# Performance work log

Hardware: AMD Instinct MI355X
Metric: run time of the kernel (lower is better)

## Reference

```python
import jax, jax.numpy as jnp
import numpy as np

WINDOW = 60
DEPTH = 3
HIDDEN = 256
LN_EPS = 1e-5


def _lyndon_indices(d):
    # Lyndon words over alphabet {0..d-1}, lengths 2 and 3, lexicographic order
    # (signatory mode='words' extracts expanded-logsig coefficients at Lyndon words).
    i2 = np.array([(i, j) for i in range(d) for j in range(d) if (i, j) < (j, i)], dtype=np.int32)
    i3 = np.array([(i, j, k) for i in range(d) for j in range(d) for k in range(d)
                   if (i, j, k) < (j, k, i) and (i, j, k) < (k, i, j)], dtype=np.int32)
    return i2, i3


def _logsig_features(x):
    # x: [b, s, c] -> logsignature of time-augmented sliding windows: [b*s, sig_channels]
    b, s, c = x.shape
    d = c + 1
    # replicate-padded sliding windows via clipped gather (matches F.pad replicate + unfold)
    pos = jnp.clip(jnp.arange(s)[:, None] + jnp.arange(WINDOW)[None, :] - (WINDOW - 1), 0, s - 1)
    windows = x[:, pos, :]                                   # [b, s, W, c]
    t = jnp.linspace(0.0, 1.0, WINDOW, dtype=x.dtype)        # time augmentation channel
    t_b = jnp.broadcast_to(t[None, None, :, None], (b, s, WINDOW, 1))
    aug = jnp.concatenate([t_b, windows], axis=-1).reshape(b * s, WINDOW, d)
    N = b * s
    # basepoint=True: prepend zero point -> increments include the first point itself
    inc = jnp.diff(aug, axis=1, prepend=jnp.zeros((N, 1, d), aug.dtype))  # [N, W, d]
    inc_t = jnp.transpose(inc, (1, 0, 2))                    # [W, N, d]

    def chen_step(carry, v):
        S1, S2, S3 = carry
        vv = jnp.einsum('ni,nj->nij', v, v)
        vvv = jnp.einsum('nij,nk->nijk', vv, v)
        nS3 = S3 + jnp.einsum('nij,nk->nijk', S2, v) \
                 + 0.5 * jnp.einsum('ni,njk->nijk', S1, vv) + vvv / 6.0
        nS2 = S2 + jnp.einsum('ni,nj->nij', S1, v) + 0.5 * vv
        nS1 = S1 + v
        return (nS1, nS2, nS3), None

    init = (jnp.zeros((N, d), x.dtype), jnp.zeros((N, d, d), x.dtype), jnp.zeros((N, d, d, d), x.dtype))
    (S1, S2, S3), _ = jax.lax.scan(chen_step, init, inc_t)
    # log in truncated tensor algebra: log(1+x) = x - x^2/2 + x^3/3
    L1 = S1
    L2 = S2 - 0.5 * jnp.einsum('ni,nj->nij', S1, S1)
    L3 = (S3 - 0.5 * (jnp.einsum('ni,njk->nijk', S1, S2) + jnp.einsum('nij,nk->nijk', S2, S1))
          + jnp.einsum('ni,nj,nk->nijk', S1, S1, S1) / 3.0)
    i2, i3 = _lyndon_indices(d)
    f2 = L2[:, i2[:, 0], i2[:, 1]]
    f3 = L3[:, i3[:, 0], i3[:, 1], i3[:, 2]]
    return jnp.concatenate([L1, f2, f3], axis=-1)            # [N, sig_channels]


def setup_inputs() -> dict:
    key = jax.random.key(0)
    ks = jax.random.split(key, 5)
    b, s, c = 8, 2048, 8
    d = c + 1
    sig_channels = d + (d * d - d) // 2 + (d ** 3 - d) // 3  # 285 for d=9
    h2 = 2 * HIDDEN
    x = jax.random.normal(ks[0], (b, s, c), dtype=jnp.float32)
    w1 = jax.random.normal(ks[1], (sig_channels, h2), dtype=jnp.float32) / np.sqrt(sig_channels)
    b1 = jnp.zeros((h2,), jnp.float32)
    ln_g = jnp.ones((h2,), jnp.float32)
    ln_b = jnp.zeros((h2,), jnp.float32)
    w2 = jax.random.normal(ks[2], (h2, HIDDEN), dtype=jnp.float32) / np.sqrt(h2)
    b2 = jnp.zeros((HIDDEN,), jnp.float32)
    return {"x": x, "w1": w1, "b1": b1, "ln_g": ln_g, "ln_b": ln_b, "w2": w2, "b2": b2}


def reference(x, w1, b1, ln_g, ln_b, w2, b2):
    b, s, _ = x.shape
    feats = _logsig_features(x)                              # [b*s, sig_channels]
    h = jax.nn.gelu(feats @ w1 + b1, approximate=False)      # torch default GELU (erf)
    mu = jnp.mean(h, axis=-1, keepdims=True)
    var = jnp.var(h, axis=-1, keepdims=True)
    h = (h - mu) / jnp.sqrt(var + LN_EPS) * ln_g + ln_b      # LayerNorm; Dropout is eval no-op
    out = h @ w2 + b2
    return out.reshape(b, s, -1)
```

## Files before the change

kernel.cpp:

```cpp
#include <hip/hip_runtime.h>
#include <hip/hip_bf16.h>
#include <cstdint>
#include <cstddef>

typedef short short8 __attribute__((ext_vector_type(8)));
typedef float f32x4 __attribute__((ext_vector_type(4)));
typedef float f32x2 __attribute__((ext_vector_type(2)));

#define NS    2048
#define KPAD  288
#define H2    512
#define HID   256
#define WPB   7
#define SBLK  293
#define SIGBLKS (8 * SBLK)

#define MFMA(a,b,c) __builtin_amdgcn_mfma_f32_16x16x32_bf16((a),(b),(c),0,0,0)

__device__ __forceinline__ void gl2lds16(const void* g, void* l) {
    __builtin_amdgcn_global_load_lds(
        (const __attribute__((address_space(1))) void*)g,
        (__attribute__((address_space(3))) void*)l, 16, 0, 0);
}
__device__ __forceinline__ float geluf(float x) {
    return 0.5f * x * (1.0f + erff(x * 0.70710678118654752f));
}
__device__ __forceinline__ f32x4 shfl4(f32x4 v, int d) {
    f32x4 r;
    r[0] = __shfl_xor(v[0], d); r[1] = __shfl_xor(v[1], d);
    r[2] = __shfl_xor(v[2], d); r[3] = __shfl_xor(v[3], d);
    return r;
}

struct Tbl3 { short col[729]; };
static constexpr Tbl3 make_tbl3() {
    Tbl3 t{};
    for (int x = 0; x < 729; ++x) t.col[x] = -1;
    int r = 0;
    for (int i = 0; i < 9; ++i)
        for (int j = 0; j < 9; ++j)
            for (int k = 0; k < 9; ++k) {
                bool lt1 = (i < j) || (i == j && (j < k || (j == k && k < i)));
                bool lt2 = (i < k) || (i == k && (j < i || (j == i && k < j)));
                if (lt1 && lt2) { t.col[(i*9+j)*9+k] = (short)(45 + r); ++r; }
            }
    return t;
}
static constexpr Tbl3 TBL3 = make_tbl3();

#define SIG_STEP(VA_,VB_,VC_) { \
    const float hh = 0.5f * S1i + vi * (1.0f/6.0f); \
    const float ra = S2ra + hh * (VA_); \
    const float rb = S2rb + hh * (VB_); \
    const float rc = S2rc + hh * (VC_); \
    const f32x2 ra2 = {ra, ra}, rb2 = {rb, rb}, rc2 = {rc, rc}; \
    S3sa += ra * v0; S3pa0 += ra2*vp0; S3pa1 += ra2*vp1; S3pa2 += ra2*vp2; S3pa3 += ra2*vp3; \
    S3sb += rb * v0; S3pb0 += rb2*vp0; S3pb1 += rb2*vp1; S3pb2 += rb2*vp2; S3pb3 += rb2*vp3; \
    S3sc += rc * v0; S3pc0 += rc2*vp0; S3pc1 += rc2*vp1; S3pc2 += rc2*vp2; S3pc3 += rc2*vp3; \
    const float aa = S1i + 0.5f * vi; \
    S2ra += aa * (VA_); S2rb += aa * (VB_); S2rc += aa * (VC_); \
    S1i += vi; }

#define SIG_DSTEP(E0,E1,RS,VA_,VB_,VC_) { \
    const float4 e0 = (E0); const float4 e1 = (E1); const float rs = (RS); \
    const float v0 = DT; \
    const f32x2 vp0 = {e0.x, e0.y}, vp1 = {e0.z, e0.w}, vp2 = {e1.x, e1.y}, vp3 = {e1.z, e1.w}; \
    const float vi = (ci == 0) ? DT : rs; \
    SIG_STEP(VA_,VB_,VC_) }

#define SIG_MAIN(VA_,VB_,VC_) { \
    { const float* xr = &X[(g0 - lo) * 8]; \
      const float4 e0 = *(const float4*)xr; \
      const float4 e1 = *(const float4*)(xr + 4); \
      const float rs = xr[ioff]; \
      const float v0 = 0.0f; \
      const f32x2 vp0 = {e0.x, e0.y}, vp1 = {e0.z, e0.w}, vp2 = {e1.x, e1.y}, vp3 = {e1.z, e1.w}; \
      const float vi = (ci == 0) ? 0.0f : rs; \
      SIG_STEP(VA_,VB_,VC_) } \
    const float* pd = &PD[(sm59 + 1 - lo + 59) * 8]; \
    float4 p0 = *(const float4*)pd; \
    float4 p1 = *(const float4*)(pd + 4); \
    float  pr = pd[ioff]; \
    float4 q0 = *(const float4*)(pd + 8); \
    float4 q1 = *(const float4*)(pd + 12); \
    float  qr = (pd + 8)[ioff]; \
    _Pragma("unroll 1") \
    for (int j = 1; j < 59; j += 2) { \
      pd += 16; \
      const float4 a0 = *(const float4*)pd; \
      const float4 a1 = *(const float4*)(pd + 4); \
      const float  ar = pd[ioff]; \
      const float4 b0 = *(const float4*)(pd + 8); \
      const float4 b1 = *(const float4*)(pd + 12); \
      const float  br = (pd + 8)[ioff]; \
      SIG_DSTEP(p0, p1, pr, VA_,VB_,VC_) \
      SIG_DSTEP(q0, q1, qr, VA_,VB_,VC_) \
      p0 = a0; p1 = a1; pr = ar; \
      q0 = b0; q1 = b1; qr = br; \
    } \
    SIG_DSTEP(p0, p1, pr, VA_,VB_,VC_) }

#define SIG_ST(RA,RB,RC) \
    if (act) { \
        if ((RA) == 0) S1buf[widx * 9 + ci] = S1i; \
        float* sb = &S2buf[widx * 81 + ci * 9]; \
        sb[RA] = S2ra; sb[RB] = S2rb; sb[RC] = S2rc; \
    }

#define S3EL0(SL) S3s##SL
#define S3EL1(SL) S3p##SL##0[0]
#define S3EL2(SL) S3p##SL##0[1]
#define S3EL3(SL) S3p##SL##1[0]
#define S3EL4(SL) S3p##SL##1[1]
#define S3EL5(SL) S3p##SL##2[0]
#define S3EL6(SL) S3p##SL##2[1]
#define S3EL7(SL) S3p##SL##3[0]
#define S3EL8(SL) S3p##SL##3[1]

#define SIG_E2(SL,J2) if (ci < (J2)) { \
    const float val2 = S2r##SL - 0.5f * S1i * s1v##J2; \
    const int col2 = 9 + ci*8 - (ci*(ci-1))/2 + ((J2) - ci - 1); \
    frow[col2] = __float2bfloat16(val2); }

#define SIG_E3(SL,R,K) { const int col3 = TBL3.col[tb + (R)*9 + (K)]; \
    if (col3 >= 0) { \
        const float val3 = S3EL##K(SL) \
            - 0.5f * (S1i * S2w[(R)*9+(K)] + S2r##SL * s1v##K) \
            + S1i * s1v##R * s1v##K * (1.0f/3.0f); \
        frow[col3] = __float2bfloat16(val3); } }

#define SIG_E3R(SL,R) SIG_E3(SL,R,0) SIG_E3(SL,R,1) SIG_E3(SL,R,2) SIG_E3(SL,R,3) \
    SIG_E3(SL,R,4) SIG_E3(SL,R,5) SIG_E3(SL,R,6) SIG_E3(SL,R,7) SIG_E3(SL,R,8)

#define SIG_EMIT(RA,RB,RC) \
    if (act) { \
        if ((RA) == 0) { \
            frow[ci] = __float2bfloat16(S1i); \
            if (ci == 0) { \
                const __hip_bfloat16 z16 = __float2bfloat16(0.0f); \
                frow[285] = z16; frow[286] = z16; frow[287] = z16; \
            } \
        } \
        SIG_E2(a,RA) SIG_E2(b,RB) SIG_E2(c,RC) \
        SIG_E3R(a,RA) SIG_E3R(b,RB) SIG_E3R(c,RC) \
    }

__global__ __launch_bounds__(192) __attribute__((amdgpu_waves_per_eu(1, 6)))
void sig_kernel(const float* __restrict__ x, __hip_bfloat16* __restrict__ feats,
                const float* __restrict__ w1, const float* __restrict__ w2,
                const float* __restrict__ lng, const float* __restrict__ lnb,
                const float* __restrict__ b2,
                __hip_bfloat16* __restrict__ w1T, __hip_bfloat16* __restrict__ w2g,
                float* __restrict__ gw, float* __restrict__ cvec) {
    __shared__ __align__(16) float X[66 * 8];
    __shared__ __align__(16) float PD[126 * 8];
    __shared__ float S2buf[WPB * 81];
    __shared__ float S1buf[WPB * 9];

    const int blk = blockIdx.x;
    const int tid = threadIdx.x;

    if (blk >= SIGBLKS) {
        const int pb = blk - SIGBLKS;
        if (pb < 256) {
            const int n = pb;
            float pa = 0.f, pc = 0.f;
            for (int k = tid; k < H2; k += 192) {
                const float wv = w2[(size_t)k * HID + n];
                const float a = lng[k] * wv;
                const float c = lnb[k] * wv;
                w2g[(size_t)n * H2 + k] = __float2bfloat16(a);
                pa += a; pc += c;
            }
#pragma unroll
            for (int d = 1; d < 64; d <<= 1) { pa += __shfl_xor(pa, d); pc += __shfl_xor(pc, d); }
            if ((tid & 63) == 0) { X[(tid >> 6) * 2] = pa; X[(tid >> 6) * 2 + 1] = pc; }
            __syncthreads();
            if (tid == 0) {
                gw[n]   = X[0] + X[2] + X[4];
                cvec[n] = X[1] + X[3] + X[5] + b2[n];
            }
        } else {
            const int n0 = (pb - 256) * 8;
            for (int e = tid; e < 8 * KPAD; e += 192) {
                const int ni = n0 + (e / KPAD);
                const int k  = e - (e / KPAD) * KPAD;
                const float v = (k < 285) ? w1[(size_t)k * H2 + ni] : 0.0f;
                w1T[(size_t)ni * KPAD + k] = __float2bfloat16(v);
            }
        }
        return;
    }

    const int b   = blk / SBLK;
    const int s0  = (blk % SBLK) * WPB;
    const int lo  = (s0 - 59 > 0) ? (s0 - 59) : 0;
    const int hi  = (s0 + WPB - 1 < NS - 1) ? (s0 + WPB - 1) : (NS - 1);
    const int nrow = hi - lo + 1;

    {
        const float4* src = (const float4*)(x + ((size_t)b * NS + lo) * 8);
        float4* X4 = (float4*)X;
        const int n4 = nrow * 2;
        for (int t = tid; t < n4; t += 192) X4[t] = src[t];
    }
    __syncthreads();
    {
        const float4* X4 = (const float4*)X;
        float4* PD4 = (float4*)PD;
        for (int t = tid; t < 252; t += 192) {
            const int p = t >> 1;
            const int r = p - 59;
            float4 dv = {0.f, 0.f, 0.f, 0.f};
            if (r > 0 && r < nrow) {
                const float4 a = X4[t - 118], bb = X4[t - 120];
                dv.x = a.x - bb.x; dv.y = a.y - bb.y; dv.z = a.z - bb.z; dv.w = a.w - bb.w;
            }
            PD4[t] = dv;
        }
    }
    __syncthreads();

    const int t3    = tid >> 6;
    const int lt    = tid & 63;
    const int widx0 = lt / 9;
    const int ci    = lt - widx0 * 9;
    const bool act  = (lt < 63) && (s0 + widx0 < NS);
    const int widx  = (widx0 < WPB - 1) ? widx0 : WPB - 1;
    int s = s0 + widx; if (s > NS - 1) s = NS - 1;

    float S3sa=0.f, S3sb=0.f, S3sc=0.f;
    f32x2 S3pa0={0.f,0.f},S3pa1={0.f,0.f},S3pa2={0.f,0.f},S3pa3={0.f,0.f};
    f32x2 S3pb0={0.f,0.f},S3pb1={0.f,0.f},S3pb2={0.f,0.f},S3pb3={0.f,0.f};
    f32x2 S3pc0={0.f,0.f},S3pc1={0.f,0.f},S3pc2={0.f,0.f},S3pc3={0.f,0.f};
    float S2ra=0.f, S2rb=0.f, S2rc=0.f;
    float S1i = 0.f;
    const int ioff = (ci > 0) ? (ci - 1) : 0;
    const int sm59 = s - 59;
    const int g0   = (sm59 > 0) ? sm59 : 0;
    const float DT = 1.0f / 59.0f;

    if (t3 == 0)      { SIG_MAIN(v0,   e0.x, e0.y) }
    else if (t3 == 1) { SIG_MAIN(e0.z, e0.w, e1.x) }
    else              { SIG_MAIN(e1.y, e1.z, e1.w) }

    if (t3 == 0)      { SIG_ST(0,1,2) }
    else if (t3 == 1) { SIG_ST(3,4,5) }
    else              { SIG_ST(6,7,8) }
    __syncthreads();

    const float* s1p = &S1buf[widx * 9];
    const float s1v0=s1p[0], s1v1=s1p[1], s1v2=s1p[2], s1v3=s1p[3], s1v4=s1p[4];
    const float s1v5=s1p[5], s1v6=s1p[6], s1v7=s1p[7], s1v8=s1p[8];
    const float* S2w = &S2buf[widx * 81];
    const int tb = ci * 81;
    __hip_bfloat16* frow = feats + (size_t)(b * NS + s) * KPAD;

    if (t3 == 0)      { SIG_EMIT(0,1,2) }
    else if (t3 == 1) { SIG_EMIT(3,4,5) }
    else              { SIG_EMIT(6,7,8) }
}

__global__ __launch_bounds__(256)
void mlp_kernel(const __hip_bfloat16* __restrict__ feats,
                const __hip_bfloat16* __restrict__ w1T,
                const float* __restrict__ bias,
                const __hip_bfloat16* __restrict__ w2g,
                const float* __restrict__ gw,
                const float* __restrict__ cvec,
                float* __restrict__ out) {
    __shared__ __align__(16) __hip_bfloat16 Blds[512 * 32];
    __shared__ __align__(16) __hip_bfloat16 Hbuf[32 * 512];
    __shared__ __align__(16) __hip_bfloat16 Ab0[32 * 32];
    __shared__ __align__(16) __hip_bfloat16 Ab1[32 * 32];
    __shared__ float sstat[4][32][2];

    const int tid  = threadIdx.x;
    const int wave = tid >> 6;
    const int lane = tid & 63;
    const int quad = lane >> 4;
    const int l16  = lane & 15;
    const int m0   = blockIdx.x * 32;
    const int swz16 = (quad ^ ((l16 >> 1) & 3)) * 16;

#define STAGE_B1(S, DST) { \
    _Pragma("unroll") \
    for (int i_ = 0; i_ < 8; ++i_) { \
        const int c_ = tid + i_ * 256; const int r_ = c_ >> 2; const int q_ = c_ & 3; \
        gl2lds16(w1T + (size_t)r_ * KPAD + (S) * 32 + ((q_ ^ ((r_ >> 1) & 3)) * 8), \
                 (char*)(DST) + (c_ & ~63) * 16); } }
#define STAGE_A(S, DST) { if (tid < 128) { \
        const int r_ = tid >> 2; const int q_ = tid & 3; \
        gl2lds16(feats + (size_t)(m0 + r_) * KPAD + (S) * 32 + ((q_ ^ ((r_ >> 1) & 3)) * 8), \
                 (char*)(DST) + (tid & ~63) * 16); } }
#define STAGE_B2(T, DST) { \
    _Pragma("unroll") \
    for (int i_ = 0; i_ < 4; ++i_) { \
        const int c_ = tid + i_ * 256; const int r_ = c_ >> 2; const int q_ = c_ & 3; \
        gl2lds16(w2g + (size_t)r_ * H2 + (T) * 32 + ((q_ ^ ((r_ >> 1) & 3)) * 8), \
                 (char*)(DST) + (c_ & ~63) * 16); } }

    ((float*)sstat)[tid] = 0.0f;
    STAGE_B1(0, Blds)
    STAGE_A(0, Ab0)
    __syncthreads();

    f32x4 a1[2][8];
#pragma unroll
    for (int mf = 0; mf < 2; ++mf)
#pragma unroll
        for (int nf = 0; nf < 8; ++nf) a1[mf][nf] = f32x4{0.f, 0.f, 0.f, 0.f};

#pragma unroll 1
    for (int s = 0; s < 9; ++s) {
        if (s < 8) {
            if ((s + 1) & 1) { STAGE_B1(s + 1, Hbuf) STAGE_A(s + 1, Ab1) }
            else             { STAGE_B1(s + 1, Blds) STAGE_A(s + 1, Ab0) }
        }
        const char* Ac = (s & 1) ? (const char*)Ab1 : (const char*)Ab0;
        const char* Bc = (s & 1) ? (const char*)Hbuf : (const char*)Blds;
        const short8 av0 = *(const short8*)(Ac + l16 * 64 + swz16);
        const short8 av1 = *(const short8*)(Ac + (16 + l16) * 64 + swz16);
#pragma unroll
        for (int nf = 0; nf < 8; ++nf) {
            const short8 bv = *(const short8*)(Bc + (size_t)(wave * 128 + nf * 16 + l16) * 64 + swz16);
            a1[0][nf] = MFMA(av0, bv, a1[0][nf]);
            a1[1][nf] = MFMA(av1, bv, a1[1][nf]);
        }
        __syncthreads();
    }

    {
        f32x4 sum0 = {0,0,0,0}, sum1 = {0,0,0,0}, sq0 = {0,0,0,0}, sq1 = {0,0,0,0};
#pragma unroll
        for (int nf = 0; nf < 8; ++nf) {
            const int col = wave * 128 + nf * 16 + l16;
            const float bv = bias[col];
            f32x4 e0, e1;
#pragma unroll
            for (int r = 0; r < 4; ++r) { e0[r] = geluf(a1[0][nf][r] + bv); e1[r] = geluf(a1[1][nf][r] + bv); }
#pragma unroll
            for (int r = 0; r < 4; ++r) {
                const int row0 = quad * 4 + r;
                const int row1 = 16 + row0;
                const int ch0 = (col >> 3) ^ (row0 & 7);
                const int ch1 = (col >> 3) ^ (row1 & 7);
                *(__hip_bfloat16*)((char*)Hbuf + row0 * 1024 + ch0 * 16 + (col & 7) * 2) = __float2bfloat16(e0[r]);
                *(__hip_bfloat16*)((char*)Hbuf + row1 * 1024 + ch1 * 16 + (col & 7) * 2) = __float2bfloat16(e1[r]);
            }
            sum0 += e0; sq0 += e0 * e0; sum1 += e1; sq1 += e1 * e1;
        }
        sum0 += shfl4(sum0, 1); sq0 += shfl4(sq0, 1); sum1 += shfl4(sum1, 1); sq1 += shfl4(sq1, 1);
        sum0 += shfl4(sum0, 2); sq0 += shfl4(sq0, 2); sum1 += shfl4(sum1, 2); sq1 += shfl4(sq1, 2);
        sum0 += shfl4(sum0, 4); sq0 += shfl4(sq0, 4); sum1 += shfl4(sum1, 4); sq1 += shfl4(sq1, 4);
        sum0 += shfl4(sum0, 8); sq0 += shfl4(sq0, 8); sum1 += shfl4(sum1, 8); sq1 += shfl4(sq1, 8);
        if (l16 == 0) {
#pragma unroll
            for (int r = 0; r < 4; ++r) {
                sstat[wave][quad * 4 + r][0]      = sum0[r];
                sstat[wave][quad * 4 + r][1]      = sq0[r];
                sstat[wave][16 + quad * 4 + r][0] = sum1[r];
                sstat[wave][16 + quad * 4 + r][1] = sq1[r];
            }
        }
        __syncthreads();
    }

    f32x4 a2[2][4];
#pragma unroll
    for (int mf = 0; mf < 2; ++mf)
#pragma unroll
        for (int nf = 0; nf < 4; ++nf) a2[mf][nf] = f32x4{0.f, 0.f, 0.f, 0.f};

    STAGE_B2(0, Blds)
    __syncthreads();

    const int hsw = l16 & 7;
#pragma unroll 1
    for (int t = 0; t < 16; ++t) {
        if (t < 15) { STAGE_B2(t + 1, (char*)Blds + ((t + 1) & 1) * 16384) }
        const char* Bc = (const char*)Blds + (t & 1) * 16384;
        const int kc = ((t * 4 + quad) ^ hsw) * 16;
        const short8 hv0 = *(const short8*)((const char*)Hbuf + l16 * 1024 + kc);
        const short8 hv1 = *(const short8*)((const char*)Hbuf + (16 + l16) * 1024 + kc);
#pragma unroll
        for (int nf = 0; nf < 4; ++nf) {
            const short8 bv = *(const short8*)(Bc + (size_t)(wave * 64 + nf * 16 + l16) * 64 + swz16);
            a2[0][nf] = MFMA(hv0, bv, a2[0][nf]);
            a2[1][nf] = MFMA(hv1, bv, a2[1][nf]);
        }
        __syncthreads();
    }

    f32x4 mu0, rs0, mu1, rs1;
#pragma unroll
    for (int r = 0; r < 4; ++r) {
        const int rl0 = quad * 4 + r, rl1 = 16 + rl0;
        const float s0 = sstat[0][rl0][0] + sstat[1][rl0][0] + sstat[2][rl0][0] + sstat[3][rl0][0];
        const float q0 = sstat[0][rl0][1] + sstat[1][rl0][1] + sstat[2][rl0][1] + sstat[3][rl0][1];
        const float s1 = sstat[0][rl1][0] + sstat[1][rl1][0] + sstat[2][rl1][0] + sstat[3][rl1][0];
        const float q1 = sstat[0][rl1][1] + sstat[1][rl1][1] + sstat[2][rl1][1] + sstat[3][rl1][1];
        mu0[r] = s0 * (1.0f / 512.0f);
        mu1[r] = s1 * (1.0f / 512.0f);
        rs0[r] = rsqrtf(q0 * (1.0f / 512.0f) - mu0[r] * mu0[r] + 1e-5f);
        rs1[r] = rsqrtf(q1 * (1.0f / 512.0f) - mu1[r] * mu1[r] + 1e-5f);
    }
#pragma unroll
    for (int nf = 0; nf < 4; ++nf) {
        const int col = wave * 64 + nf * 16 + l16;
        const float g_ = gw[col], c_ = cvec[col];
#pragma unroll
        for (int r = 0; r < 4; ++r) {
            const int row0 = m0 + quad * 4 + r;
            const int row1 = row0 + 16;
            out[(size_t)row0 * HID + col] = rs0[r] * (a2[0][nf][r] - mu0[r] * g_) + c_;
            out[(size_t)row1 * HID + col] = rs1[r] * (a2[1][nf][r] - mu1[r] * g_) + c_;
        }
    }
}

extern "C" void kernel_launch(void* const* d_in, const int* in_sizes, int n_in,
                              void* d_out, int out_size, void* d_ws, size_t ws_size,
                              hipStream_t stream) {
    const float* x   = (const float*)d_in[0];
    const float* w1  = (const float*)d_in[1];
    const float* b1  = (const float*)d_in[2];
    const float* lng = (const float*)d_in[3];
    const float* lnb = (const float*)d_in[4];
    const float* w2  = (const float*)d_in[5];
    const float* b2  = (const float*)d_in[6];
    float* out = (float*)d_out;

    char* ws = (char*)d_ws;
    __hip_bfloat16* feats = (__hip_bfloat16*)(ws);
    __hip_bfloat16* w1T   = (__hip_bfloat16*)(ws + 9437184);
    __hip_bfloat16* w2g   = (__hip_bfloat16*)(ws + 9732096);
    float*          gw    = (float*)(ws + 9994240);
    float*          cvec  = (float*)(ws + 9995264);

    sig_kernel<<<dim3(SIGBLKS + 320), dim3(192), 0, stream>>>(
        x, feats, w1, w2, lng, lnb, b2, w1T, w2g, gw, cvec);
    mlp_kernel<<<dim3(512), dim3(256), 0, stream>>>(feats, w1T, b1, w2g, gw, cvec, out);
}
```

Before: 146.6 us.

## Share 56-step signature core across 4 adjacent windows via Chen combination

Each wave slot now handles a segment of four consecutive windows. It computes the signature of the 56 shared increments once, then for each window builds a short head and tail prefix and combines them with Chen's identity. Previously each window scanned all 60 steps on its own. This cuts redundant per-step arithmetic roughly fourfold. In exchange it adds more registers (a second signature set), per-window syncthreads and LDS round-trips, and fewer, larger blocks.

```diff
diff --git a/kernel.cpp b/kernel.cpp
--- a/kernel.cpp
+++ b/kernel.cpp
@@ -11,8 +11,10 @@
 #define KPAD  288
 #define H2    512
 #define HID   256
-#define WPB   7
-#define SBLK  293
+#define WIN   4
+#define SEGS  7
+#define WPB   28
+#define SBLK  74
 #define SIGBLKS (8 * SBLK)
 
 #define MFMA(a,b,c) __builtin_amdgcn_mfma_f32_16x16x32_bf16((a),(b),(c),0,0,0)
@@ -31,6 +33,7 @@
     r[2] = __shfl_xor(v[2], d); r[3] = __shfl_xor(v[3], d);
     return r;
 }
+__device__ __forceinline__ f32x2 mk2(float a, float b) { f32x2 r; r[0] = a; r[1] = b; return r; }
 
 struct Tbl3 { short col[729]; };
 static constexpr Tbl3 make_tbl3() {
@@ -48,64 +51,88 @@
 }
 static constexpr Tbl3 TBL3 = make_tbl3();
 
-#define SIG_STEP(VA_,VB_,VC_) { \
-    const float hh = 0.5f * S1i + vi * (1.0f/6.0f); \
-    const float ra = S2ra + hh * (VA_); \
-    const float rb = S2rb + hh * (VB_); \
-    const float rc = S2rc + hh * (VC_); \
+#define SIG_STEPX(P,VA_,VB_,VC_) { \
+    const float hh = 0.5f * S1i##P + vi * (1.0f/6.0f); \
+    const float ra = S2ra##P + hh * (VA_); \
+    const float rb = S2rb##P + hh * (VB_); \
+    const float rc = S2rc##P + hh * (VC_); \
     const f32x2 ra2 = {ra, ra}, rb2 = {rb, rb}, rc2 = {rc, rc}; \
-    S3sa += ra * v0; S3pa0 += ra2*vp0; S3pa1 += ra2*vp1; S3pa2 += ra2*vp2; S3pa3 += ra2*vp3; \
-    S3sb += rb * v0; S3pb0 += rb2*vp0; S3pb1 += rb2*vp1; S3pb2 += rb2*vp2; S3pb3 += rb2*vp3; \
-    S3sc += rc * v0; S3pc0 += rc2*vp0; S3pc1 += rc2*vp1; S3pc2 += rc2*vp2; S3pc3 += rc2*vp3; \
-    const float aa = S1i + 0.5f * vi; \
-    S2ra += aa * (VA_); S2rb += aa * (VB_); S2rc += aa * (VC_); \
-    S1i += vi; }
-
-#define SIG_DSTEP(E0,E1,RS,VA_,VB_,VC_) { \
-    const float4 e0 = (E0); const float4 e1 = (E1); const float rs = (RS); \
+    S3sa##P += ra * v0; S3pa0##P += ra2*vp0; S3pa1##P += ra2*vp1; S3pa2##P += ra2*vp2; S3pa3##P += ra2*vp3; \
+    S3sb##P += rb * v0; S3pb0##P += rb2*vp0; S3pb1##P += rb2*vp1; S3pb2##P += rb2*vp2; S3pb3##P += rb2*vp3; \
+    S3sc##P += rc * v0; S3pc0##P += rc2*vp0; S3pc1##P += rc2*vp1; S3pc2##P += rc2*vp2; S3pc3##P += rc2*vp3; \
+    const float aa = S1i##P + 0.5f * vi; \
+    S2ra##P += aa * (VA_); S2rb##P += aa * (VB_); S2rc##P += aa * (VC_); \
+    S1i##P += vi; }
+
+#define DIFF_STEPR(PR,VA_,VB_,VC_) { \
+    const float* pr_ = (PR); \
+    const float4 e0 = *(const float4*)pr_; \
+    const float4 e1 = *(const float4*)(pr_ + 4); \
+    const float rs = pr_[ioff]; \
     const float v0 = DT; \
     const f32x2 vp0 = {e0.x, e0.y}, vp1 = {e0.z, e0.w}, vp2 = {e1.x, e1.y}, vp3 = {e1.z, e1.w}; \
     const float vi = (ci == 0) ? DT : rs; \
-    SIG_STEP(VA_,VB_,VC_) }
-
-#define SIG_MAIN(VA_,VB_,VC_) { \
-    { const float* xr = &X[(g0 - lo) * 8]; \
+    SIG_STEPX(R,VA_,VB_,VC_) }
+
+#define DIFF_STEPL(PR,VA_,VB_,VC_) { \
+    const float* pr_ = (PR); \
+    const float4 e0 = *(const float4*)pr_; \
+    const float4 e1 = *(const float4*)(pr_ + 4); \
+    const float rs = pr_[ioff]; \
+    const float v0 = DT; \
+    const f32x2 vp0 = {e0.x, e0.y}, vp1 = {e0.z, e0.w}, vp2 = {e1.x, e1.y}, vp3 = {e1.z, e1.w}; \
+    const float vi = (ci == 0) ? DT : rs; \
+    SIG_STEPX(,VA_,VB_,VC_) }
+
+#define CORE56(VA_,VB_,VC_) { \
+    const float* pdc = &PD[(A0 - 55) * 8]; \
+    _Pragma("unroll 2") \
+    for (int i_ = 0; i_ < 56; ++i_) { DIFF_STEPR(pdc, VA_,VB_,VC_) pdc += 8; } }
+
+#define PHA(RA,RB,RC,VA_,VB_,VC_) { \
+    if (j > 0) DIFF_STEPR(&PD[(A0 + j) * 8], VA_,VB_,VC_) \
+    { const float* xr = &X[g0l * 8]; \
       const float4 e0 = *(const float4*)xr; \
       const float4 e1 = *(const float4*)(xr + 4); \
       const float rs = xr[ioff]; \
       const float v0 = 0.0f; \
       const f32x2 vp0 = {e0.x, e0.y}, vp1 = {e0.z, e0.w}, vp2 = {e1.x, e1.y}, vp3 = {e1.z, e1.w}; \
       const float vi = (ci == 0) ? 0.0f : rs; \
-      SIG_STEP(VA_,VB_,VC_) } \
-    const float* pd = &PD[(sm59 + 1 - lo + 59) * 8]; \
-    float4 p0 = *(const float4*)pd; \
-    float4 p1 = *(const float4*)(pd + 4); \
-    float  pr = pd[ioff]; \
-    float4 q0 = *(const float4*)(pd + 8); \
-    float4 q1 = *(const float4*)(pd + 12); \
-    float  qr = (pd + 8)[ioff]; \
-    _Pragma("unroll 1") \
-    for (int j = 1; j < 59; j += 2) { \
-      pd += 16; \
-      const float4 a0 = *(const float4*)pd; \
-      const float4 a1 = *(const float4*)(pd + 4); \
-      const float  ar = pd[ioff]; \
-      const float4 b0 = *(const float4*)(pd + 8); \
-      const float4 b1 = *(const float4*)(pd + 12); \
-      const float  br = (pd + 8)[ioff]; \
-      SIG_DSTEP(p0, p1, pr, VA_,VB_,VC_) \
-      SIG_DSTEP(q0, q1, qr, VA_,VB_,VC_) \
-      p0 = a0; p1 = a1; pr = ar; \
-      q0 = b0; q1 = b1; qr = br; \
-    } \
-    SIG_DSTEP(p0, p1, pr, VA_,VB_,VC_) }
-
-#define SIG_ST(RA,RB,RC) \
-    if (act) { \
-        if ((RA) == 0) S1buf[widx * 9 + ci] = S1i; \
-        float* sb = &S2buf[widx * 81 + ci * 9]; \
-        sb[RA] = S2ra; sb[RB] = S2rb; sb[RC] = S2rc; \
-    }
+      SIG_STEPX(,VA_,VB_,VC_) } \
+    { const float* pm = &PD[(A0 + j - 58) * 8]; \
+      for (int i2 = 0; i2 < 3 - j; ++i2) { DIFF_STEPL(pm, VA_,VB_,VC_) pm += 8; } } \
+    if (lt < 63) { \
+        if ((RA) == 0) R1buf[seg * 9 + ci] = S1iR; \
+        float* rb_ = &R2buf[seg * 81 + ci * 9]; \
+        rb_[RA] = S2raR; rb_[RB] = S2rbR; rb_[RC] = S2rcR; } }
+
+#define SIG_CMP(SL,M) { \
+    const float* rr = &R2buf[seg * 81 + (M) * 9]; \
+    const f32x2 l2q = {S2r##SL, S2r##SL}; \
+    S3s##SL   += S1i * rr[0] + S2r##SL * r1_0 + S3s##SL##R; \
+    S3p##SL##0 += s1i2 * mk2(rr[1], rr[2]) + l2q * r1q0 + S3p##SL##0R; \
+    S3p##SL##1 += s1i2 * mk2(rr[3], rr[4]) + l2q * r1q1 + S3p##SL##1R; \
+    S3p##SL##2 += s1i2 * mk2(rr[5], rr[6]) + l2q * r1q2 + S3p##SL##2R; \
+    S3p##SL##3 += s1i2 * mk2(rr[7], rr[8]) + l2q * r1q3 + S3p##SL##3R; }
+
+#define R1V(M) r1_##M
+
+#define PHB(RA,RB,RC) { \
+    const float* r1p = &R1buf[seg * 9]; \
+    const float r1_0=r1p[0], r1_1=r1p[1], r1_2=r1p[2], r1_3=r1p[3], r1_4=r1p[4]; \
+    const float r1_5=r1p[5], r1_6=r1p[6], r1_7=r1p[7], r1_8=r1p[8]; \
+    const f32x2 s1i2 = {S1i, S1i}; \
+    const f32x2 r1q0 = mk2(r1_1, r1_2), r1q1 = mk2(r1_3, r1_4); \
+    const f32x2 r1q2 = mk2(r1_5, r1_6), r1q3 = mk2(r1_7, r1_8); \
+    SIG_CMP(a,RA) SIG_CMP(b,RB) SIG_CMP(c,RC) \
+    S2ra += S1i * R1V(RA) + S2raR; \
+    S2rb += S1i * R1V(RB) + S2rbR; \
+    S2rc += S1i * R1V(RC) + S2rcR; \
+    S1i += S1iR; \
+    if (lt < 63) { \
+        if ((RA) == 0) W1buf[seg * 9 + ci] = S1i; \
+        float* wb_ = &W2buf[seg * 81 + ci * 9]; \
+        wb_[RA] = S2ra; wb_[RB] = S2rb; wb_[RC] = S2rc; } }
 
 #define S3EL0(SL) S3s##SL
 #define S3EL1(SL) S3p##SL##0[0]
@@ -145,17 +172,28 @@
         SIG_E3R(a,RA) SIG_E3R(b,RB) SIG_E3R(c,RC) \
     }
 
-__global__ __launch_bounds__(192) __attribute__((amdgpu_waves_per_eu(1, 6)))
+#define PHC(RA,RB,RC) { \
+    const float* s1p = &W1buf[seg * 9]; \
+    const float s1v0=s1p[0], s1v1=s1p[1], s1v2=s1p[2], s1v3=s1p[3], s1v4=s1p[4]; \
+    const float s1v5=s1p[5], s1v6=s1p[6], s1v7=s1p[7], s1v8=s1p[8]; \
+    const float* S2w = &W2buf[seg * 81]; \
+    const int tb = ci * 81; \
+    __hip_bfloat16* frow = feats + (size_t)(b * NS + wj) * KPAD; \
+    SIG_EMIT(RA,RB,RC) }
+
+__global__ __launch_bounds__(192) __attribute__((amdgpu_waves_per_eu(1, 4)))
 void sig_kernel(const float* __restrict__ x, __hip_bfloat16* __restrict__ feats,
                 const float* __restrict__ w1, const float* __restrict__ w2,
                 const float* __restrict__ lng, const float* __restrict__ lnb,
                 const float* __restrict__ b2,
                 __hip_bfloat16* __restrict__ w1T, __hip_bfloat16* __restrict__ w2g,
                 float* __restrict__ gw, float* __restrict__ cvec) {
-    __shared__ __align__(16) float X[66 * 8];
-    __shared__ __align__(16) float PD[126 * 8];
-    __shared__ float S2buf[WPB * 81];
-    __shared__ float S1buf[WPB * 9];
+    __shared__ __align__(16) float X[87 * 8];
+    __shared__ __align__(16) float PD[146 * 8];
+    __shared__ float R1buf[SEGS * 9];
+    __shared__ float R2buf[SEGS * 81];
+    __shared__ float W1buf[SEGS * 9];
+    __shared__ float W2buf[SEGS * 81];
 
     const int blk = blockIdx.x;
     const int tid = threadIdx.x;
@@ -208,7 +246,7 @@
     {
         const float4* X4 = (const float4*)X;
         float4* PD4 = (float4*)PD;
-        for (int t = tid; t < 252; t += 192) {
+        for (int t = tid; t < 292; t += 192) {
             const int p = t >> 1;
             const int r = p - 59;
             float4 dv = {0.f, 0.f, 0.f, 0.f};
@@ -225,40 +263,51 @@
     const int lt    = tid & 63;
     const int widx0 = lt / 9;
     const int ci    = lt - widx0 * 9;
-    const bool act  = (lt < 63) && (s0 + widx0 < NS);
-    const int widx  = (widx0 < WPB - 1) ? widx0 : WPB - 1;
-    int s = s0 + widx; if (s > NS - 1) s = NS - 1;
-
-    float S3sa=0.f, S3sb=0.f, S3sc=0.f;
-    f32x2 S3pa0={0.f,0.f},S3pa1={0.f,0.f},S3pa2={0.f,0.f},S3pa3={0.f,0.f};
-    f32x2 S3pb0={0.f,0.f},S3pb1={0.f,0.f},S3pb2={0.f,0.f},S3pb3={0.f,0.f};
-    f32x2 S3pc0={0.f,0.f},S3pc1={0.f,0.f},S3pc2={0.f,0.f},S3pc3={0.f,0.f};
-    float S2ra=0.f, S2rb=0.f, S2rc=0.f;
-    float S1i = 0.f;
-    const int ioff = (ci > 0) ? (ci - 1) : 0;
-    const int sm59 = s - 59;
-    const int g0   = (sm59 > 0) ? sm59 : 0;
-    const float DT = 1.0f / 59.0f;
-
-    if (t3 == 0)      { SIG_MAIN(v0,   e0.x, e0.y) }
-    else if (t3 == 1) { SIG_MAIN(e0.z, e0.w, e1.x) }
-    else              { SIG_MAIN(e1.y, e1.z, e1.w) }
-
-    if (t3 == 0)      { SIG_ST(0,1,2) }
-    else if (t3 == 1) { SIG_ST(3,4,5) }
-    else              { SIG_ST(6,7,8) }
-    __syncthreads();
-
-    const float* s1p = &S1buf[widx * 9];
-    const float s1v0=s1p[0], s1v1=s1p[1], s1v2=s1p[2], s1v3=s1p[3], s1v4=s1p[4];
-    const float s1v5=s1p[5], s1v6=s1p[6], s1v7=s1p[7], s1v8=s1p[8];
-    const float* S2w = &S2buf[widx * 81];
-    const int tb = ci * 81;
-    __hip_bfloat16* frow = feats + (size_t)(b * NS + s) * KPAD;
-
-    if (t3 == 0)      { SIG_EMIT(0,1,2) }
-    else if (t3 == 1) { SIG_EMIT(3,4,5) }
-    else              { SIG_EMIT(6,7,8) }
+    const int seg   = (widx0 < SEGS) ? widx0 : SEGS - 1;
+    const int wbase = s0 + seg * WIN;
+    const int A0    = 59 + (wbase - lo);
+    const int ioff  = (ci > 0) ? (ci - 1) : 0;
+    const float DT  = 1.0f / 59.0f;
+
+    float S1iR = 0.f, S2raR = 0.f, S2rbR = 0.f, S2rcR = 0.f;
+    float S3saR = 0.f, S3sbR = 0.f, S3scR = 0.f;
+    f32x2 S3pa0R={0,0},S3pa1R={0,0},S3pa2R={0,0},S3pa3R={0,0};
+    f32x2 S3pb0R={0,0},S3pb1R={0,0},S3pb2R={0,0},S3pb3R={0,0};
+    f32x2 S3pc0R={0,0},S3pc1R={0,0},S3pc2R={0,0},S3pc3R={0,0};
+    float S1i, S2ra, S2rb, S2rc, S3sa, S3sb, S3sc;
+    f32x2 S3pa0,S3pa1,S3pa2,S3pa3,S3pb0,S3pb1,S3pb2,S3pb3,S3pc0,S3pc1,S3pc2,S3pc3;
+
+    if (t3 == 0)      { CORE56(v0,   e0.x, e0.y) }
+    else if (t3 == 1) { CORE56(e0.z, e0.w, e1.x) }
+    else              { CORE56(e1.y, e1.z, e1.w) }
+
+#pragma unroll 1
+    for (int j = 0; j < WIN; ++j) {
+        const int wj  = wbase + j;
+        const bool act = (lt < 63) && (wj < NS);
+        int g0 = wj - 59; if (g0 < 0) g0 = 0;
+        const int g0l = g0 - lo;
+
+        S1i = 0.f; S2ra = 0.f; S2rb = 0.f; S2rc = 0.f;
+        S3sa = 0.f; S3sb = 0.f; S3sc = 0.f;
+        S3pa0 = mk2(0,0); S3pa1 = mk2(0,0); S3pa2 = mk2(0,0); S3pa3 = mk2(0,0);
+        S3pb0 = mk2(0,0); S3pb1 = mk2(0,0); S3pb2 = mk2(0,0); S3pb3 = mk2(0,0);
+        S3pc0 = mk2(0,0); S3pc1 = mk2(0,0); S3pc2 = mk2(0,0); S3pc3 = mk2(0,0);
+
+        if (t3 == 0)      { PHA(0,1,2, v0,   e0.x, e0.y) }
+        else if (t3 == 1) { PHA(3,4,5, e0.z, e0.w, e1.x) }
+        else              { PHA(6,7,8, e1.y, e1.z, e1.w) }
+        __syncthreads();
+
+        if (t3 == 0)      { PHB(0,1,2) }
+        else if (t3 == 1) { PHB(3,4,5) }
+        else              { PHB(6,7,8) }
+        __syncthreads();
+
+        if (t3 == 0)      { PHC(0,1,2) }
+        else if (t3 == 1) { PHC(3,4,5) }
+        else              { PHC(6,7,8) }
+    }
 }
 
 __global__ __launch_bounds__(256)
```

Result: no change. 147.8 us (+0.8%).
